# Performance work log

Measured on AMD Instinct MI355X. Metric: run time of the kernel, lower is better.

Reference implementation:

```python
import jax, jax.numpy as jnp
import numpy as np

EPS = 1e-5
TAU = 2.0

# Heaviside spike with spikingjelly's default Sigmoid surrogate gradient (alpha=4)
@jax.custom_vjp
def spike(x):
    return (x >= 0.0).astype(x.dtype)

def _spike_fwd(x):
    return (x >= 0.0).astype(x.dtype), x

def _spike_bwd(x, g):
    a = 4.0
    s = jax.nn.sigmoid(a * x)
    return (g * a * s * (1.0 - s),)

spike.defvjp(_spike_fwd, _spike_bwd)

def lif(x_seq, v_th, v_reset):
    """Multi-step LIF (decay_input=True, detach_reset=True). v_reset=None -> soft reset."""
    def step(v, x):
        if v_reset is None:
            v = v + (x - v) / TAU
        else:
            v = v + (x - (v - v_reset)) / TAU
        s = spike(v - v_th)
        sd = jax.lax.stop_gradient(s)  # detach_reset=True
        if v_reset is None:
            v = v - sd * v_th
        else:
            v = (1.0 - sd) * v + sd * v_reset
        return v, s
    _, s_seq = jax.lax.scan(step, jnp.zeros_like(x_seq[0]), x_seq)
    return s_seq

def conv2d(x, w, groups=1):
    return jax.lax.conv_general_dilated(x, w, (1, 1), 'VALID',
        dimension_numbers=('NCHW', 'OIHW', 'NCHW'), feature_group_count=groups)

def bn(x, p):
    # p: [4, C] = (weight, bias, running_mean, running_var); inference-mode BN
    w, b, m, v = p
    inv = w * jax.lax.rsqrt(v + EPS)
    return x * inv[None, :, None, None] + (b - m * inv)[None, :, None, None]

def bn_pad(x, p):
    # BNAndPadLayer(pad_pixels=1): BN then pad 1px border with the BN of zeros
    y = bn(x, p)
    w, b, m, v = p
    pv = (b - m * w * jax.lax.rsqrt(v + EPS))[None, :, None, None]
    y = jnp.pad(y, ((0, 0), (0, 0), (1, 1), (1, 1)))
    y = y.at[:, :, :1, :].set(pv)
    y = y.at[:, :, -1:, :].set(pv)
    y = y.at[:, :, :, :1].set(pv)
    y = y.at[:, :, :, -1:].set(pv)
    return y

def repconv(x, w1, bn1, dw, pw, bn2):
    y = conv2d(x, w1)                       # 1x1 in->in
    y = bn_pad(y, bn1)                      # BN + 1px pad
    y = conv2d(y, dw, groups=dw.shape[0])   # depthwise 3x3, valid
    y = conv2d(y, pw)                       # 1x1 in->out
    return bn(y, bn2)

def setup_inputs() -> dict:
    T, B, C, H, W = 4, 16, 384, 32, 32
    key = jax.random.key(0)
    ks = iter(jax.random.split(key, 32))
    def bn_params(c):
        k1, k2, k3, k4 = jax.random.split(next(ks), 4)
        return jnp.stack([
            1.0 + 0.1 * jax.random.normal(k1, (c,)),
            0.1 * jax.random.normal(k2, (c,)),
            0.1 * jax.random.normal(k3, (c,)),
            jax.random.uniform(k4, (c,), minval=0.5, maxval=1.5)]).astype(jnp.float32)
    def conv_w(shape, fan_in):
        return (jax.random.normal(next(ks), shape) / np.sqrt(fan_in)).astype(jnp.float32)
    return dict(
        x=jax.random.normal(next(ks), (T, B, C, H, W), dtype=jnp.float32),
        r1_w1=conv_w((C, C, 1, 1), C),
        r1_bn1=bn_params(C),
        r1_dw=conv_w((C, 1, 3, 3), 9),
        r1_pw=conv_w((2 * C, C, 1, 1), C),
        r1_bn2=bn_params(2 * C),
        qkv_bn=bn_params(2 * C),
        r2_w1=conv_w((C, C, 1, 1), C),
        r2_bn1=bn_params(C),
        r2_dw=conv_w((C, 1, 3, 3), 9),
        r2_pw=conv_w((C, C, 1, 1), C),
        r2_bn2=bn_params(C),
        proj_bn=bn_params(C),
        scale=jnp.array([0.1], dtype=jnp.float32),
    )

def reference(x, r1_w1, r1_bn1, r1_dw, r1_pw, r1_bn2, qkv_bn,
              r2_w1, r2_bn1, r2_dw, r2_pw, r2_bn2, proj_bn, scale):
    T, B, C, H, W = x.shape
    xs = lif(x, 1.0, 0.0)                                  # shortcut_lif (hard reset)
    y = repconv(xs.reshape(T * B, C, H, W), r1_w1, r1_bn1, r1_dw, r1_pw, r1_bn2)
    y = bn(y, qkv_bn).reshape(T, B, 2 * C, H, W)           # qkv_conv outer BN
    qk, v = y[:, :, :C], y[:, :, C:]
    qk = lif(qk, 1.0, None)                                # qk_lif (soft reset)
    qk = qk.sum(axis=(-1, -2), keepdims=True)              # jit_sum over H,W -> [T,B,C,1,1]
    qk = lif(qk, 0.5, 0.0)                                 # talking_heads_lif (th=0.5, hard)
    v = lif(v, 1.0, None)                                  # v_lif (soft reset)
    out = qk * v                                           # jit_mul broadcast over H,W
    out = repconv(out.reshape(T * B, C, H, W), r2_w1, r2_bn1, r2_dw, r2_pw, r2_bn2)
    out = bn(out, proj_bn).reshape(T, B, C, H, W)          # proj_conv outer BN
    out = lif(out, 1.0, None)                              # proj_lif (soft reset)
    return out * scale
```

## Files before the change

### kernel.cpp

```cpp
#include <hip/hip_runtime.h>

typedef _Float16 f16;
typedef __attribute__((ext_vector_type(8))) _Float16 f16x8;
typedef __attribute__((ext_vector_type(4))) _Float16 f16x4;
typedef __attribute__((ext_vector_type(4))) float f32x4;

#define TT 4
#define BB 16
#define CC 384

#define SWZ(R) ((((R) & 31)) ^ ((((R) & 4)) << 2))

__device__ __forceinline__ float lif_soft(float x, float& v) {
  v = __fadd_rn(v, __fmul_rn(__fsub_rn(x, v), 0.5f));
  float s = (__fsub_rn(v, 1.0f) >= 0.0f) ? 1.0f : 0.0f;
  v = __fsub_rn(v, s);
  return s;
}
__device__ __forceinline__ float lif_hard(float x, float& v, float vth) {
  v = __fadd_rn(v, __fmul_rn(__fsub_rn(x, v), 0.5f));
  float s = (__fsub_rn(v, vth) >= 0.0f) ? 1.0f : 0.0f;
  if (s != 0.0f) v = 0.0f;
  return s;
}

__global__ __launch_bounds__(768) void k_prep(const float* __restrict__ bn1,
                                              const float* __restrict__ bn2,
                                              const float* __restrict__ qkv,
                                              const float* __restrict__ rbn1,
                                              const float* __restrict__ rbn2,
                                              const float* __restrict__ proj,
                                              float* __restrict__ par) {
  int c = threadIdx.x;
  float* s1 = par;          float* o1 = par + 384;
  float* sA = par + 768;    float* oA = par + 1536;
  float* s2 = par + 2304;   float* o2 = par + 2688;
  float* sB = par + 3072;   float* oB = par + 3456;
  if (c < 384) {
    double a = (double)bn1[c] / sqrt((double)bn1[3*384+c] + 1e-5);
    s1[c] = (float)a;
    o1[c] = (float)((double)bn1[384+c] - (double)bn1[2*384+c]*a);
    double a2 = (double)rbn1[c] / sqrt((double)rbn1[3*384+c] + 1e-5);
    s2[c] = (float)a2;
    o2[c] = (float)((double)rbn1[384+c] - (double)rbn1[2*384+c]*a2);
    double a3 = (double)rbn2[c] / sqrt((double)rbn2[3*384+c] + 1e-5);
    double b3 = (double)rbn2[384+c] - (double)rbn2[2*384+c]*a3;
    double a4 = (double)proj[c] / sqrt((double)proj[3*384+c] + 1e-5);
    double b4 = (double)proj[384+c] - (double)proj[2*384+c]*a4;
    sB[c] = (float)(a3*a4);
    oB[c] = (float)(b3*a4 + b4);
  }
  if (c < 768) {
    double a5 = (double)bn2[c] / sqrt((double)bn2[3*768+c] + 1e-5);
    double b5 = (double)bn2[768+c] - (double)bn2[2*768+c]*a5;
    double a6 = (double)qkv[c] / sqrt((double)qkv[3*768+c] + 1e-5);
    double b6 = (double)qkv[768+c] - (double)qkv[2*768+c]*a6;
    sA[c] = (float)(a5*a6);
    oA[c] = (float)(b5*a6 + b6);
  }
}

__global__ __launch_bounds__(256) void k_wsplit(const float* __restrict__ w,
                                                f16* __restrict__ wa, f16* __restrict__ wb, int n) {
  int i = blockIdx.x * 256 + threadIdx.x;
  if (i < n) {
    float x = w[i];
    f16 a = (f16)x;
    wa[i] = a;
    wb[i] = (f16)((x - (float)a) * 2048.0f);
  }
}

__global__ __launch_bounds__(256) void k_lif_in(const float* __restrict__ x, f16* __restrict__ xs) {
  __shared__ float tile[64][65];
  const int p0 = blockIdx.x * 64, c0 = blockIdx.y * 64, b = blockIdx.z;
  const int l = threadIdx.x & 63, q = threadIdx.x >> 6;
  float v[16];
  #pragma unroll
  for (int j = 0; j < 16; ++j) v[j] = 0.0f;
  for (int t = 0; t < TT; ++t) {
    __syncthreads();
    #pragma unroll
    for (int j = 0; j < 16; ++j) {
      int ci = q + j*4;
      tile[ci][l] = x[(((size_t)(t*BB + b)*CC + c0 + ci) << 10) + p0 + l];
    }
    __syncthreads();
    #pragma unroll
    for (int j = 0; j < 16; ++j) {
      int pi = q + j*4;
      float s = lif_hard(tile[l][pi], v[j], 1.0f);
      xs[((size_t)(t*BB + b)*1024 + p0 + pi)*CC + c0 + l] = (f16)s;
    }
  }
}

template<int EPI>
__device__ __forceinline__ void stage_arrT(const f16* __restrict__ g, int m0, int b_, int p0,
                                           int k0, f16* dst, int lane, int i0, int i1, bool isX) {
  #pragma unroll
  for (int i = i0; i < i1; ++i) {
    int loff = i*1024 + lane*16;
    int row = loff >> 6, col = loff & 63;
    int scol = col ^ (((row >> 1) & 3) << 4);
    int gm;
    if (EPI >= 1 && isX) gm = ((row >> 5) << 14) + (b_ << 10) + p0 + (row & 31);
    else                 gm = m0 + row;
    const char* src = (const char*)g + (size_t)gm*768 + (size_t)(k0*2) + scol;
    __builtin_amdgcn_global_load_lds((const __attribute__((address_space(1))) void*)src,
                                     (__attribute__((address_space(3))) void*)((char*)dst + i*1024),
                                     16, 0, 0);
  }
}

__device__ __forceinline__ f16x8 fragld32(const f16* arr, int row, int fq) {
  int off = row*64 + ((fq*16) ^ (((row >> 1) & 3) << 4));
  return *(const f16x8*)((const char*)arr + off);
}

template<int NP, int EPI, int GATE>
__global__ __launch_bounds__(256, 2) void k_gemm(const f16* __restrict__ X1, const f16* __restrict__ X2,
    const f16* __restrict__ Wa, const f16* __restrict__ Wb,
    const float* __restrict__ scale, const float* __restrict__ bias,
    float* __restrict__ out0, const float* __restrict__ out1,
    const f16* __restrict__ gatep, f16* __restrict__ sOut, f16* __restrict__ part) {
  constexpr int ARR = (NP == 3) ? 4 : 3;
  __shared__ __align__(16) f16 lds[2*ARR*4096];
  const int gx = gridDim.x;
  const int bid = blockIdx.y * gx + blockIdx.x;
  const int chunk = (gx * gridDim.y) >> 3;
  const int nb = (bid & 7) * chunk + (bid >> 3);
  const int o0 = (nb % gx) * 128;
  const int mb = nb / gx;
  const int m0 = mb * 128;
  const int b_ = mb >> 5, p0 = (mb & 31) << 5;
  const int lane = threadIdx.x & 63, wid = threadIdx.x >> 6;
  const int wr = wid >> 1, wc = wid & 1;
  const int fr = lane & 15, fq = lane >> 4;
  f32x4 acc_h[4][4], acc_l[4][4];
  #pragma unroll
  for (int i = 0; i < 4; ++i)
    #pragma unroll
    for (int j = 0; j < 4; ++j) { acc_h[i][j] = (f32x4){0,0,0,0}; acc_l[i][j] = (f32x4){0,0,0,0}; }

  auto stage_all = [&](int buf, int k0) {
    f16* base = lds + buf*(ARR*4096);
    if (NP == 3) {
      if (wid == 0)      stage_arrT<EPI>(X1, m0, b_, p0, k0, base,          lane, 0, 8, true);
      else if (wid == 1) stage_arrT<EPI>(X2, m0, b_, p0, k0, base + 4096,   lane, 0, 8, true);
      else if (wid == 2) stage_arrT<EPI>(Wa, o0, b_, p0, k0, base + 2*4096, lane, 0, 8, false);
      else               stage_arrT<EPI>(Wb, o0, b_, p0, k0, base + 3*4096, lane, 0, 8, false);
    } else {
      if (wid == 0)      stage_arrT<EPI>(X1, m0, b_, p0, k0, base,          lane, 0, 4, true);
      else if (wid == 1) stage_arrT<EPI>(X1, m0, b_, p0, k0, base,          lane, 4, 8, true);
      else if (wid == 2) stage_arrT<EPI>(Wa, o0, b_, p0, k0, base + 4096,   lane, 0, 8, false);
      else               stage_arrT<EPI>(Wb, o0, b_, p0, k0, base + 2*4096, lane, 0, 8, false);
    }
  };

  const char* gbase = nullptr;
  f16x8 g8{}, gn{};
  if constexpr (GATE) {
    gbase = (const char*)gatep + (size_t)(m0 >> 10)*768 + fq*16;
    g8 = *(const f16x8*)gbase;
  }

  stage_all(0, 0);
  __syncthreads();

  for (int it = 0; it < 12; ++it) {
    const int cur = it & 1;
    if (it < 11) stage_all(cur ^ 1, (it + 1)*32);
    if constexpr (GATE) { if (it < 11) gn = *(const f16x8*)(gbase + (it + 1)*64); }
    const f16* bX1 = lds + cur*(ARR*4096);
    const f16* bW1 = (NP == 3) ? bX1 + 2*4096 : bX1 + 4096;
    const f16* bW2 = (NP == 3) ? bX1 + 3*4096 : bX1 + 2*4096;
    f16x8 a1[4], b1[4], b2[4];
    #pragma unroll
    for (int mi = 0; mi < 4; ++mi) a1[mi] = fragld32(bX1, wr*64 + mi*16 + fr, fq);
    if constexpr (GATE) {
      #pragma unroll
      for (int mi = 0; mi < 4; ++mi) a1[mi] = a1[mi] * g8;
    }
    #pragma unroll
    for (int oi = 0; oi < 4; ++oi) {
      b1[oi] = fragld32(bW1, wc*64 + oi*16 + fr, fq);
      b2[oi] = fragld32(bW2, wc*64 + oi*16 + fr, fq);
    }
    if (NP == 3) {
      const f16* bX2 = bX1 + 4096;
      f16x8 a2[4];
      #pragma unroll
      for (int mi = 0; mi < 4; ++mi) a2[mi] = fragld32(bX2, wr*64 + mi*16 + fr, fq);
      #pragma unroll
      for (int mi = 0; mi < 4; ++mi)
        #pragma unroll
        for (int oi = 0; oi < 4; ++oi) {
          acc_h[mi][oi] = __builtin_amdgcn_mfma_f32_16x16x32_f16(a1[mi], b1[oi], acc_h[mi][oi], 0, 0, 0);
          acc_l[mi][oi] = __builtin_amdgcn_mfma_f32_16x16x32_f16(a1[mi], b2[oi], acc_l[mi][oi], 0, 0, 0);
          acc_l[mi][oi] = __builtin_amdgcn_mfma_f32_16x16x32_f16(a2[mi], b1[oi], acc_l[mi][oi], 0, 0, 0);
        }
    } else {
      #pragma unroll
      for (int mi = 0; mi < 4; ++mi)
        #pragma unroll
        for (int oi = 0; oi < 4; ++oi) {
          acc_h[mi][oi] = __builtin_amdgcn_mfma_f32_16x16x32_f16(a1[mi], b1[oi], acc_h[mi][oi], 0, 0, 0);
          acc_l[mi][oi] = __builtin_amdgcn_mfma_f32_16x16x32_f16(a1[mi], b2[oi], acc_l[mi][oi], 0, 0, 0);
        }
    }
    __syncthreads();
    if constexpr (GATE) { if (it < 11) g8 = gn; }
  }

  if constexpr (EPI == 0) {
    #pragma unroll
    for (int oi = 0; oi < 4; ++oi) {
      int o = o0 + wc*64 + oi*16 + fr;
      float sc = scale[o], bi = bias[o];
      #pragma unroll
      for (int mi = 0; mi < 4; ++mi) {
        f32x4 h = acc_h[mi][oi], lo2 = acc_l[mi][oi];
        #pragma unroll
        for (int r = 0; r < 4; ++r) {
          int m = m0 + wr*64 + mi*16 + fq*4 + r;
          float y = fmaf(0.00048828125f, lo2[r], h[r]);
          out0[(size_t)m*384 + o] = fmaf(y, sc, bi);
        }
      }
    }
  } else {
    float* T = (float*)lds;
    #pragma unroll
    for (int oi = 0; oi < 4; ++oi) {
      int ol = wc*64 + oi*16 + fr;
      float sc = scale[o0 + ol], bi = bias[o0 + ol];
      #pragma unroll
      for (int mi = 0; mi < 4; ++mi) {
        f32x4 h = acc_h[mi][oi], lo2 = acc_l[mi][oi];
        #pragma unroll
        for (int r = 0; r < 4; ++r) {
          int R = wr*64 + mi*16 + fq*4 + r;
          float y = fmaf(0.00048828125f, lo2[r], h[r]);
          T[R*128 + (ol ^ SWZ(R))] = fmaf(y, sc, bi);
        }
      }
    }
    __syncthreads();
    const int tid = threadIdx.x;
    if constexpr (EPI == 1) {
      const int oc = tid & 127, ph = tid >> 7;
      if (o0 >= 384) {
        const int ocg = (o0 - 384) + oc;
        #pragma unroll
        for (int i = 0; i < 16; ++i) {
          int p = ph*16 + i;
          float v = 0.0f;
          #pragma unroll
          for (int t = 0; t < TT; ++t) {
            int R = t*32 + p;
            float s = lif_soft(T[R*128 + (oc ^ SWZ(R))], v);
            sOut[((size_t)((t*16 + b_)*1024 + p0 + p))*384 + ocg] = (f16)s;
          }
        }
      } else {
        float ps4[4] = {0,0,0,0};
        for (int i = 0; i < 16; ++i) {
          int p = ph*16 + i;
          float v = 0.0f;
          #pragma unroll
          for (int t = 0; t < TT; ++t) {
            int R = t*32 + p;
            ps4[t] += lif_soft(T[R*128 + (oc ^ SWZ(R))], v);
          }
        }
        int slice = (p0 >> 4) + ph;
        #pragma unroll
        for (int t = 0; t < TT; ++t)
          part[(((size_t)slice*4 + t)*16 + b_)*384 + o0 + oc] = (f16)ps4[t];
      }
    } else {
      const int p = tid & 31, cg = tid >> 5;
      const float gsc = out1[0];
      #pragma unroll
      for (int j = 0; j < 16; ++j) {
        int c = cg*16 + j;
        float v = 0.0f;
        #pragma unroll
        for (int t = 0; t < TT; ++t) {
          int R = t*32 + p;
          float s = lif_soft(T[R*128 + (c ^ SWZ(R))], v) * gsc;
          out0[(((size_t)(t*16 + b_)*384) + o0 + c)*1024 + p0 + p] = s;
        }
      }
    }
  }
}

__global__ __launch_bounds__(256) void k_dw(const float* __restrict__ in, const float* __restrict__ wd,
                                            const float* __restrict__ pv,
                                            f16* __restrict__ outA, f16* __restrict__ outB) {
  const int ct = blockIdx.x, h = blockIdx.y, n = blockIdx.z;
  const int cq = threadIdx.x & 15, wg = threadIdx.x >> 4;
  const int c0 = ct*64 + cq*4;
  const int w0 = wg*2;
  float w9[9][4];
  #pragma unroll
  for (int j = 0; j < 4; ++j)
    #pragma unroll
    for (int k = 0; k < 9; ++k) w9[k][j] = wd[(c0 + j)*9 + k];
  const float4 pv4 = *(const float4*)&pv[c0];
  const float* base = in + (size_t)n*1024*CC;
  float4 col[3][4];
  #pragma unroll
  for (int r = 0; r < 3; ++r)
    #pragma unroll
    for (int j = 0; j < 4; ++j) {
      int hh = h - 1 + r, ww = w0 - 1 + j;
      col[r][j] = ((unsigned)hh < 32u && (unsigned)ww < 32u)
                  ? *(const float4*)&base[(size_t)(hh*32 + ww)*CC + c0] : pv4;
    }
  #pragma unroll
  for (int wi = 0; wi < 2; ++wi) {
    float acc[4] = {0.f, 0.f, 0.f, 0.f};
    #pragma unroll
    for (int dh = 0; dh < 3; ++dh)
      #pragma unroll
      for (int dwj = 0; dwj < 3; ++dwj) {
        float4 vv = col[dh][wi + dwj];
        const float* wk = w9[dh*3 + dwj];
        acc[0] = fmaf(wk[0], vv.x, acc[0]);
        acc[1] = fmaf(wk[1], vv.y, acc[1]);
        acc[2] = fmaf(wk[2], vv.z, acc[2]);
        acc[3] = fmaf(wk[3], vv.w, acc[3]);
      }
    f16x4 a4, b4;
    #pragma unroll
    for (int j = 0; j < 4; ++j) {
      f16 a = (f16)acc[j];
      a4[j] = a;
      b4[j] = (f16)((acc[j] - (float)a) * 2048.0f);
    }
    size_t off = ((size_t)n*1024 + h*32 + w0 + wi)*CC + c0;
    *(f16x4*)&outA[off] = a4;
    *(f16x4*)&outB[off] = b4;
  }
}

__global__ __launch_bounds__(256) void k_gate(const f16* __restrict__ partial, f16* __restrict__ gate16) {
  int g = blockIdx.x*256 + threadIdx.x;
  int b = g / CC, c = g % CC;
  float sums[4];
  #pragma unroll
  for (int t = 0; t < TT; ++t) {
    float s = 0.0f;
    for (int ps = 0; ps < 64; ++ps) s += (float)partial[(((size_t)ps*4 + t)*BB + b)*CC + c];
    sums[t] = s;
  }
  float v = 0.0f;
  #pragma unroll
  for (int t = 0; t < TT; ++t)
    gate16[((size_t)(t*BB + b))*CC + c] = (f16)lif_hard(sums[t], v, 0.5f);
}

extern "C" void kernel_launch(void* const* d_in, const int* in_sizes, int n_in,
                              void* d_out, int out_size, void* d_ws, size_t ws_size,
                              hipStream_t stream) {
  const float* x      = (const float*)d_in[0];
  const float* r1_w1  = (const float*)d_in[1];
  const float* r1_bn1 = (const float*)d_in[2];
  const float* r1_dw  = (const float*)d_in[3];
  const float* r1_pw  = (const float*)d_in[4];
  const float* r1_bn2 = (const float*)d_in[5];
  const float* qkv_bn = (const float*)d_in[6];
  const float* r2_w1  = (const float*)d_in[7];
  const float* r2_bn1 = (const float*)d_in[8];
  const float* r2_dw  = (const float*)d_in[9];
  const float* r2_pw  = (const float*)d_in[10];
  const float* r2_bn2 = (const float*)d_in[11];
  const float* proj_bn= (const float*)d_in[12];
  const float* scale  = (const float*)d_in[13];

  float* ws = (float*)d_ws;
  const size_t SEG = 12582912;
  float* W0f = ws;
  float* W1  = ws + SEG;
  float* W2f = ws + 3*SEG;
  float* W3  = ws + 4*SEG;
  f16* xs  = (f16*)W0f;
  f16* p1a = (f16*)W0f;
  f16* p2b = (f16*)W0f;
  f16* p1b = (f16*)W2f;
  f16* p2a = (f16*)W2f;
  float* t1  = W1;
  f16*  s16  = (f16*)W1;
  float* t2  = W3;

  f16* wsp = (f16*)(ws + 6*SEG);
  f16* w1a = wsp,              *w1b = wsp + 147456;
  f16* pwa = wsp + 294912,     *pwb = wsp + 589824;
  f16* q1a = wsp + 884736,     *q1b = wsp + 1032192;
  f16* qpa = wsp + 1179648,    *qpb = wsp + 1327104;
  f16* partial = wsp + 1474560;
  f16* gate16  = wsp + 3047424;
  float* par = (float*)(wsp + 3072000);
  float* s1 = par,        *o1 = par + 384;
  float* sA = par + 768,  *oA = par + 1536;
  float* s2 = par + 2304, *o2 = par + 2688;
  float* sB = par + 3072, *oB = par + 3456;

  const f16* nf = (const f16*)nullptr;
  f16* nf2 = (f16*)nullptr;

  k_prep<<<1, 768, 0, stream>>>(r1_bn1, r1_bn2, qkv_bn, r2_bn1, r2_bn2, proj_bn, par);
  k_wsplit<<<576, 256, 0, stream>>>(r1_w1, w1a, w1b, 147456);
  k_wsplit<<<1152, 256, 0, stream>>>(r1_pw, pwa, pwb, 294912);
  k_wsplit<<<576, 256, 0, stream>>>(r2_w1, q1a, q1b, 147456);
  k_wsplit<<<576, 256, 0, stream>>>(r2_pw, qpa, qpb, 147456);
  k_lif_in<<<dim3(16, 6, 16), 256, 0, stream>>>(x, xs);
  k_gemm<2,0,0><<<dim3(3, 512), 256, 0, stream>>>(xs, nf, w1a, w1b, s1, o1, t1, nullptr, nf, nf2, nf2);
  k_dw<<<dim3(6, 32, 64), 256, 0, stream>>>(t1, r1_dw, o1, p1a, p1b);
  k_gemm<3,1,0><<<dim3(6, 512), 256, 0, stream>>>(p1a, p1b, pwa, pwb, sA, oA,
                                                  nullptr, nullptr, nf, s16, partial);
  k_gate<<<24, 256, 0, stream>>>(partial, gate16);
  k_gemm<2,0,1><<<dim3(3, 512), 256, 0, stream>>>(s16, nf, q1a, q1b, s2, o2, t2, nullptr, gate16, nf2, nf2);
  k_dw<<<dim3(6, 32, 64), 256, 0, stream>>>(t2, r2_dw, o2, p2a, p2b);
  k_gemm<3,2,0><<<dim3(3, 512), 256, 0, stream>>>(p2a, p2b, qpa, qpb, sB, oB,
                                                  (float*)d_out, scale, nf, nf2, nf2);
}
```

Baseline: 514.7 us.

## Split GEMM into specialized kernels with precomputed pointers and direct X2 register loads

Replaces the templated GEMM with two specialized kernels. Both precompute the global-to-LDS source pointers and fragment offsets and unroll the double-buffered k-loop by two. The three-operand variant now reads the low-part activation (X2) straight from global memory into registers instead of staging it in LDS, which cuts LDS traffic and the LDS footprint to 64KB. The four weight-split launches and the BN parameter prep are merged into one kernel, and workspace buffers are reassigned. The risk is higher register pressure and uncoalesced global loads for X2.

After: 526.4 us. 1.02x slower.

```diff
diff --git a/kernel.cpp b/kernel.cpp
--- a/kernel.cpp
+++ b/kernel.cpp
@@ -24,14 +24,28 @@
   return s;
 }
 
-__global__ __launch_bounds__(768) void k_prep(const float* __restrict__ bn1,
-                                              const float* __restrict__ bn2,
-                                              const float* __restrict__ qkv,
-                                              const float* __restrict__ rbn1,
-                                              const float* __restrict__ rbn2,
-                                              const float* __restrict__ proj,
-                                              float* __restrict__ par) {
-  int c = threadIdx.x;
+__global__ __launch_bounds__(256) void k_prep_all(const float* __restrict__ w1, const float* __restrict__ pw,
+    const float* __restrict__ q1, const float* __restrict__ qp,
+    f16* __restrict__ w1a, f16* __restrict__ w1b, f16* __restrict__ pwa, f16* __restrict__ pwb,
+    f16* __restrict__ q1a, f16* __restrict__ q1b, f16* __restrict__ qpa, f16* __restrict__ qpb,
+    const float* __restrict__ bn1, const float* __restrict__ bn2, const float* __restrict__ qkv,
+    const float* __restrict__ rbn1, const float* __restrict__ rbn2, const float* __restrict__ proj,
+    float* __restrict__ par) {
+  int bid = blockIdx.x;
+  if (bid < 2880) {
+    int i = bid*256 + threadIdx.x;
+    const float* s; f16 *da, *db; int idx;
+    if (i < 147456)      { s = w1; da = w1a; db = w1b; idx = i; }
+    else if (i < 442368) { s = pw; da = pwa; db = pwb; idx = i - 147456; }
+    else if (i < 589824) { s = q1; da = q1a; db = q1b; idx = i - 442368; }
+    else                 { s = qp; da = qpa; db = qpb; idx = i - 589824; }
+    float x = s[idx];
+    f16 a = (f16)x;
+    da[idx] = a;
+    db[idx] = (f16)((x - (float)a) * 2048.0f);
+    return;
+  }
+  int c = (bid - 2880)*256 + threadIdx.x;
   float* s1 = par;          float* o1 = par + 384;
   float* sA = par + 768;    float* oA = par + 1536;
   float* s2 = par + 2304;   float* o2 = par + 2688;
@@ -60,17 +74,6 @@
   }
 }
 
-__global__ __launch_bounds__(256) void k_wsplit(const float* __restrict__ w,
-                                                f16* __restrict__ wa, f16* __restrict__ wb, int n) {
-  int i = blockIdx.x * 256 + threadIdx.x;
-  if (i < n) {
-    float x = w[i];
-    f16 a = (f16)x;
-    wa[i] = a;
-    wb[i] = (f16)((x - (float)a) * 2048.0f);
-  }
-}
-
 __global__ __launch_bounds__(256) void k_lif_in(const float* __restrict__ x, f16* __restrict__ xs) {
   __shared__ float tile[64][65];
   const int p0 = blockIdx.x * 64, c0 = blockIdx.y * 64, b = blockIdx.z;
@@ -95,44 +98,132 @@
   }
 }
 
-template<int EPI>
-__device__ __forceinline__ void stage_arrT(const f16* __restrict__ g, int m0, int b_, int p0,
-                                           int k0, f16* dst, int lane, int i0, int i1, bool isX) {
-  #pragma unroll
-  for (int i = i0; i < i1; ++i) {
+__device__ __forceinline__ int fragoff(int row, int fq) {
+  return row*64 + ((fq*16) ^ (((row >> 1) & 3) << 4));
+}
+
+#define GLL(srcP, dstP) __builtin_amdgcn_global_load_lds( \
+    (const __attribute__((address_space(1))) void*)(srcP), \
+    (__attribute__((address_space(3))) void*)(dstP), 16, 0, 0)
+
+template<int GATE>
+__global__ __launch_bounds__(256, 2) void k_gemmA(const f16* __restrict__ X1,
+    const f16* __restrict__ Wa, const f16* __restrict__ Wb,
+    const float* __restrict__ scale, const float* __restrict__ bias,
+    float* __restrict__ out0, const f16* __restrict__ gatep) {
+  __shared__ __align__(16) f16 lds[2*3*4096];
+  char* lbase = (char*)lds;
+  const int gx = gridDim.x;
+  const int bid = blockIdx.y * gx + blockIdx.x;
+  const int chunk = (gx * gridDim.y) >> 3;
+  const int nb = (bid & 7) * chunk + (bid >> 3);
+  const int o0 = (nb % gx) * 128;
+  const int m0 = (nb / gx) * 128;
+  const int lane = threadIdx.x & 63, wid = threadIdx.x >> 6;
+  const int wr = wid >> 1, wc = wid & 1;
+  const int fr = lane & 15, fq = lane >> 4;
+  f32x4 acc_h[4][4], acc_l[4][4];
+  #pragma unroll
+  for (int i = 0; i < 4; ++i)
+    #pragma unroll
+    for (int j = 0; j < 4; ++j) { acc_h[i][j] = (f32x4){0,0,0,0}; acc_l[i][j] = (f32x4){0,0,0,0}; }
+
+  const f16* gp; int i0, nst, arr, row0;
+  if (wid == 0)      { gp = X1; arr = 0; i0 = 0; nst = 4; row0 = m0; }
+  else if (wid == 1) { gp = X1; arr = 0; i0 = 4; nst = 4; row0 = m0; }
+  else if (wid == 2) { gp = Wa; arr = 1; i0 = 0; nst = 8; row0 = o0; }
+  else               { gp = Wb; arr = 2; i0 = 0; nst = 8; row0 = o0; }
+  const char* srcp[8]; int dsto[8];
+  #pragma unroll
+  for (int j = 0; j < 8; ++j) {
+    int i = i0 + (j < nst ? j : 0);
     int loff = i*1024 + lane*16;
     int row = loff >> 6, col = loff & 63;
     int scol = col ^ (((row >> 1) & 3) << 4);
-    int gm;
-    if (EPI >= 1 && isX) gm = ((row >> 5) << 14) + (b_ << 10) + p0 + (row & 31);
-    else                 gm = m0 + row;
-    const char* src = (const char*)g + (size_t)gm*768 + (size_t)(k0*2) + scol;
-    __builtin_amdgcn_global_load_lds((const __attribute__((address_space(1))) void*)src,
-                                     (__attribute__((address_space(3))) void*)((char*)dst + i*1024),
-                                     16, 0, 0);
-  }
-}
-
-__device__ __forceinline__ f16x8 fragld32(const f16* arr, int row, int fq) {
-  int off = row*64 + ((fq*16) ^ (((row >> 1) & 3) << 4));
-  return *(const f16x8*)((const char*)arr + off);
-}
-
-template<int NP, int EPI, int GATE>
-__global__ __launch_bounds__(256, 2) void k_gemm(const f16* __restrict__ X1, const f16* __restrict__ X2,
+    srcp[j] = (const char*)gp + (size_t)(row0 + row)*768 + scol;
+    dsto[j] = arr*8192 + i*1024;
+  }
+  int offA[4], offB1[4], offB2[4];
+  #pragma unroll
+  for (int mi = 0; mi < 4; ++mi) offA[mi] = fragoff(wr*64 + mi*16 + fr, fq);
+  #pragma unroll
+  for (int oi = 0; oi < 4; ++oi) {
+    int o = fragoff(wc*64 + oi*16 + fr, fq);
+    offB1[oi] = 8192 + o;
+    offB2[oi] = 16384 + o;
+  }
+
+  const char* gb = nullptr; f16x8 gcur{}, gnxt{};
+  if constexpr (GATE) {
+    gb = (const char*)gatep + (size_t)(m0 >> 10)*768 + fq*16;
+    gcur = *(const f16x8*)gb; gb += 64;
+  }
+
+#define ISSUE_A(BUF) { _Pragma("unroll") for (int j = 0; j < 8; ++j) if (j < nst) { \
+    GLL(srcp[j], lbase + (BUF) + dsto[j]); srcp[j] += 64; } }
+#define COMPUTE_A(BUF) { f16x8 a1[4], b1[4], b2[4]; \
+    _Pragma("unroll") for (int mi = 0; mi < 4; ++mi) { \
+      a1[mi] = *(const f16x8*)(lbase + (BUF) + offA[mi]); \
+      if constexpr (GATE) a1[mi] = a1[mi] * gcur; } \
+    _Pragma("unroll") for (int oi = 0; oi < 4; ++oi) { \
+      b1[oi] = *(const f16x8*)(lbase + (BUF) + offB1[oi]); \
+      b2[oi] = *(const f16x8*)(lbase + (BUF) + offB2[oi]); } \
+    _Pragma("unroll") for (int mi = 0; mi < 4; ++mi) \
+      _Pragma("unroll") for (int oi = 0; oi < 4; ++oi) { \
+        acc_h[mi][oi] = __builtin_amdgcn_mfma_f32_16x16x32_f16(a1[mi], b1[oi], acc_h[mi][oi], 0, 0, 0); \
+        acc_l[mi][oi] = __builtin_amdgcn_mfma_f32_16x16x32_f16(a1[mi], b2[oi], acc_l[mi][oi], 0, 0, 0); } }
+
+  ISSUE_A(0);
+  __syncthreads();
+  #pragma unroll 1
+  for (int it2 = 0; it2 < 6; ++it2) {
+    ISSUE_A(24576);
+    if constexpr (GATE) { gnxt = *(const f16x8*)gb; gb += 64; }
+    COMPUTE_A(0);
+    if constexpr (GATE) gcur = gnxt;
+    __syncthreads();
+    if (it2 < 5) {
+      ISSUE_A(0);
+      if constexpr (GATE) { gnxt = *(const f16x8*)gb; gb += 64; }
+    }
+    COMPUTE_A(24576);
+    if constexpr (GATE) gcur = gnxt;
+    __syncthreads();
+  }
+#undef ISSUE_A
+#undef COMPUTE_A
+
+  #pragma unroll
+  for (int oi = 0; oi < 4; ++oi) {
+    int o = o0 + wc*64 + oi*16 + fr;
+    float sc = scale[o], bi = bias[o];
+    #pragma unroll
+    for (int mi = 0; mi < 4; ++mi) {
+      f32x4 h = acc_h[mi][oi], lo2 = acc_l[mi][oi];
+      #pragma unroll
+      for (int r = 0; r < 4; ++r) {
+        int m = m0 + wr*64 + mi*16 + fq*4 + r;
+        float y = fmaf(0.00048828125f, lo2[r], h[r]);
+        out0[(size_t)m*384 + o] = fmaf(y, sc, bi);
+      }
+    }
+  }
+}
+
+template<int EPI>
+__global__ __launch_bounds__(256, 2) void k_gemmB(const f16* __restrict__ X1, const f16* __restrict__ X2,
     const f16* __restrict__ Wa, const f16* __restrict__ Wb,
     const float* __restrict__ scale, const float* __restrict__ bias,
-    float* __restrict__ out0, const float* __restrict__ out1,
-    const f16* __restrict__ gatep, f16* __restrict__ sOut, f16* __restrict__ part) {
-  constexpr int ARR = (NP == 3) ? 4 : 3;
-  __shared__ __align__(16) f16 lds[2*ARR*4096];
+    float* __restrict__ outF, const float* __restrict__ gscale,
+    f16* __restrict__ sOut, f16* __restrict__ part) {
+  __shared__ __align__(16) f16 lds[32768];
+  char* lbase = (char*)lds;
   const int gx = gridDim.x;
   const int bid = blockIdx.y * gx + blockIdx.x;
   const int chunk = (gx * gridDim.y) >> 3;
   const int nb = (bid & 7) * chunk + (bid >> 3);
   const int o0 = (nb % gx) * 128;
   const int mb = nb / gx;
-  const int m0 = mb * 128;
   const int b_ = mb >> 5, p0 = (mb & 31) << 5;
   const int lane = threadIdx.x & 63, wid = threadIdx.x >> 6;
   const int wr = wid >> 1, wc = wid & 1;
@@ -143,155 +234,139 @@
     #pragma unroll
     for (int j = 0; j < 4; ++j) { acc_h[i][j] = (f32x4){0,0,0,0}; acc_l[i][j] = (f32x4){0,0,0,0}; }
 
-  auto stage_all = [&](int buf, int k0) {
-    f16* base = lds + buf*(ARR*4096);
-    if (NP == 3) {
-      if (wid == 0)      stage_arrT<EPI>(X1, m0, b_, p0, k0, base,          lane, 0, 8, true);
-      else if (wid == 1) stage_arrT<EPI>(X2, m0, b_, p0, k0, base + 4096,   lane, 0, 8, true);
-      else if (wid == 2) stage_arrT<EPI>(Wa, o0, b_, p0, k0, base + 2*4096, lane, 0, 8, false);
-      else               stage_arrT<EPI>(Wb, o0, b_, p0, k0, base + 3*4096, lane, 0, 8, false);
-    } else {
-      if (wid == 0)      stage_arrT<EPI>(X1, m0, b_, p0, k0, base,          lane, 0, 4, true);
-      else if (wid == 1) stage_arrT<EPI>(X1, m0, b_, p0, k0, base,          lane, 4, 8, true);
-      else if (wid == 2) stage_arrT<EPI>(Wa, o0, b_, p0, k0, base + 4096,   lane, 0, 8, false);
-      else               stage_arrT<EPI>(Wb, o0, b_, p0, k0, base + 2*4096, lane, 0, 8, false);
-    }
-  };
-
-  const char* gbase = nullptr;
-  f16x8 g8{}, gn{};
-  if constexpr (GATE) {
-    gbase = (const char*)gatep + (size_t)(m0 >> 10)*768 + fq*16;
-    g8 = *(const f16x8*)gbase;
-  }
-
-  stage_all(0, 0);
+  const char* srcp[6]; int dsto[6];
+  #pragma unroll
+  for (int j = 0; j < 6; ++j) {
+    int s = wid*6 + j, arr = s >> 3, inst = s & 7;
+    int loff = inst*1024 + lane*16;
+    int row = loff >> 6, col = loff & 63;
+    int scol = col ^ (((row >> 1) & 3) << 4);
+    const f16* gp = (arr == 0) ? X1 : (arr == 1) ? Wa : Wb;
+    int gm = (arr == 0) ? (((row >> 5) << 14) + (b_ << 10) + p0 + (row & 31)) : (o0 + row);
+    srcp[j] = (const char*)gp + (size_t)gm*768 + scol;
+    dsto[j] = arr*8192 + inst*1024;
+  }
+  const char* a2p[4];
+  #pragma unroll
+  for (int mi = 0; mi < 4; ++mi) {
+    int R = wr*64 + mi*16 + fr;
+    int gm2 = ((R >> 5) << 14) + (b_ << 10) + p0 + (R & 31);
+    a2p[mi] = (const char*)X2 + (size_t)gm2*768 + fq*16;
+  }
+  int offA[4], offB1[4], offB2[4];
+  #pragma unroll
+  for (int mi = 0; mi < 4; ++mi) offA[mi] = fragoff(wr*64 + mi*16 + fr, fq);
+  #pragma unroll
+  for (int oi = 0; oi < 4; ++oi) {
+    int o = fragoff(wc*64 + oi*16 + fr, fq);
+    offB1[oi] = 8192 + o;
+    offB2[oi] = 16384 + o;
+  }
+
+  f16x8 a2c[4], a2n[4];
+
+#define ISSUE_B(BUF) { _Pragma("unroll") for (int j = 0; j < 6; ++j) { \
+    GLL(srcp[j], lbase + (BUF) + dsto[j]); srcp[j] += 64; } }
+#define LOADA2N { _Pragma("unroll") for (int mi = 0; mi < 4; ++mi) { \
+    a2n[mi] = *(const f16x8*)a2p[mi]; a2p[mi] += 64; } }
+#define COMPUTE_B(BUF) { f16x8 a1[4], b1[4], b2[4]; \
+    _Pragma("unroll") for (int mi = 0; mi < 4; ++mi) \
+      a1[mi] = *(const f16x8*)(lbase + (BUF) + offA[mi]); \
+    _Pragma("unroll") for (int oi = 0; oi < 4; ++oi) { \
+      b1[oi] = *(const f16x8*)(lbase + (BUF) + offB1[oi]); \
+      b2[oi] = *(const f16x8*)(lbase + (BUF) + offB2[oi]); } \
+    _Pragma("unroll") for (int mi = 0; mi < 4; ++mi) \
+      _Pragma("unroll") for (int oi = 0; oi < 4; ++oi) { \
+        acc_h[mi][oi] = __builtin_amdgcn_mfma_f32_16x16x32_f16(a1[mi], b1[oi], acc_h[mi][oi], 0, 0, 0); \
+        acc_l[mi][oi] = __builtin_amdgcn_mfma_f32_16x16x32_f16(a1[mi], b2[oi], acc_l[mi][oi], 0, 0, 0); \
+        acc_l[mi][oi] = __builtin_amdgcn_mfma_f32_16x16x32_f16(a2c[mi], b1[oi], acc_l[mi][oi], 0, 0, 0); } }
+
+  ISSUE_B(0);
+  #pragma unroll
+  for (int mi = 0; mi < 4; ++mi) { a2c[mi] = *(const f16x8*)a2p[mi]; a2p[mi] += 64; }
   __syncthreads();
-
-  for (int it = 0; it < 12; ++it) {
-    const int cur = it & 1;
-    if (it < 11) stage_all(cur ^ 1, (it + 1)*32);
-    if constexpr (GATE) { if (it < 11) gn = *(const f16x8*)(gbase + (it + 1)*64); }
-    const f16* bX1 = lds + cur*(ARR*4096);
-    const f16* bW1 = (NP == 3) ? bX1 + 2*4096 : bX1 + 4096;
-    const f16* bW2 = (NP == 3) ? bX1 + 3*4096 : bX1 + 2*4096;
-    f16x8 a1[4], b1[4], b2[4];
-    #pragma unroll
-    for (int mi = 0; mi < 4; ++mi) a1[mi] = fragld32(bX1, wr*64 + mi*16 + fr, fq);
-    if constexpr (GATE) {
+  #pragma unroll 1
+  for (int it2 = 0; it2 < 6; ++it2) {
+    ISSUE_B(24576);
+    LOADA2N;
+    COMPUTE_B(0);
+    #pragma unroll
+    for (int mi = 0; mi < 4; ++mi) a2c[mi] = a2n[mi];
+    __syncthreads();
+    if (it2 < 5) {
+      ISSUE_B(0);
+      LOADA2N;
+    }
+    COMPUTE_B(24576);
+    #pragma unroll
+    for (int mi = 0; mi < 4; ++mi) a2c[mi] = a2n[mi];
+    __syncthreads();
+  }
+#undef ISSUE_B
+#undef LOADA2N
+#undef COMPUTE_B
+
+  float* T = (float*)lds;
+  #pragma unroll
+  for (int oi = 0; oi < 4; ++oi) {
+    int ol = wc*64 + oi*16 + fr;
+    float sc = scale[o0 + ol], bi = bias[o0 + ol];
+    #pragma unroll
+    for (int mi = 0; mi < 4; ++mi) {
+      f32x4 h = acc_h[mi][oi], lo2 = acc_l[mi][oi];
       #pragma unroll
-      for (int mi = 0; mi < 4; ++mi) a1[mi] = a1[mi] * g8;
-    }
-    #pragma unroll
-    for (int oi = 0; oi < 4; ++oi) {
-      b1[oi] = fragld32(bW1, wc*64 + oi*16 + fr, fq);
-      b2[oi] = fragld32(bW2, wc*64 + oi*16 + fr, fq);
-    }
-    if (NP == 3) {
-      const f16* bX2 = bX1 + 4096;
-      f16x8 a2[4];
+      for (int r = 0; r < 4; ++r) {
+        int R = wr*64 + mi*16 + fq*4 + r;
+        float y = fmaf(0.00048828125f, lo2[r], h[r]);
+        T[R*128 + (ol ^ SWZ(R))] = fmaf(y, sc, bi);
+      }
+    }
+  }
+  __syncthreads();
+  const int tid = threadIdx.x;
+  if constexpr (EPI == 1) {
+    const int oc = tid & 127, ph = tid >> 7;
+    if (o0 >= 384) {
+      const int ocg = (o0 - 384) + oc;
       #pragma unroll
-      for (int mi = 0; mi < 4; ++mi) a2[mi] = fragld32(bX2, wr*64 + mi*16 + fr, fq);
-      #pragma unroll
-      for (int mi = 0; mi < 4; ++mi)
-        #pragma unroll
-        for (int oi = 0; oi < 4; ++oi) {
-          acc_h[mi][oi] = __builtin_amdgcn_mfma_f32_16x16x32_f16(a1[mi], b1[oi], acc_h[mi][oi], 0, 0, 0);
-          acc_l[mi][oi] = __builtin_amdgcn_mfma_f32_16x16x32_f16(a1[mi], b2[oi], acc_l[mi][oi], 0, 0, 0);
-          acc_l[mi][oi] = __builtin_amdgcn_mfma_f32_16x16x32_f16(a2[mi], b1[oi], acc_l[mi][oi], 0, 0, 0);
-        }
-    } else {
-      #pragma unroll
-      for (int mi = 0; mi < 4; ++mi)
-        #pragma unroll
-        for (int oi = 0; oi < 4; ++oi) {
-          acc_h[mi][oi] = __builtin_amdgcn_mfma_f32_16x16x32_f16(a1[mi], b1[oi], acc_h[mi][oi], 0, 0, 0);
-          acc_l[mi][oi] = __builtin_amdgcn_mfma_f32_16x16x32_f16(a1[mi], b2[oi], acc_l[mi][oi], 0, 0, 0);
-        }
-    }
-    __syncthreads();
-    if constexpr (GATE) { if (it < 11) g8 = gn; }
-  }
-
-  if constexpr (EPI == 0) {
-    #pragma unroll
-    for (int oi = 0; oi < 4; ++oi) {
-      int o = o0 + wc*64 + oi*16 + fr;
-      float sc = scale[o], bi = bias[o];
-      #pragma unroll
-      for (int mi = 0; mi < 4; ++mi) {
-        f32x4 h = acc_h[mi][oi], lo2 = acc_l[mi][oi];
-        #pragma unroll
-        for (int r = 0; r < 4; ++r) {
-          int m = m0 + wr*64 + mi*16 + fq*4 + r;
-          float y = fmaf(0.00048828125f, lo2[r], h[r]);
-          out0[(size_t)m*384 + o] = fmaf(y, sc, bi);
-        }
-      }
-    }
-  } else {
-    float* T = (float*)lds;
-    #pragma unroll
-    for (int oi = 0; oi < 4; ++oi) {
-      int ol = wc*64 + oi*16 + fr;
-      float sc = scale[o0 + ol], bi = bias[o0 + ol];
-      #pragma unroll
-      for (int mi = 0; mi < 4; ++mi) {
-        f32x4 h = acc_h[mi][oi], lo2 = acc_l[mi][oi];
-        #pragma unroll
-        for (int r = 0; r < 4; ++r) {
-          int R = wr*64 + mi*16 + fq*4 + r;
-          float y = fmaf(0.00048828125f, lo2[r], h[r]);
-          T[R*128 + (ol ^ SWZ(R))] = fmaf(y, sc, bi);
-        }
-      }
-    }
-    __syncthreads();
-    const int tid = threadIdx.x;
-    if constexpr (EPI == 1) {
-      const int oc = tid & 127, ph = tid >> 7;
-      if (o0 >= 384) {
-        const int ocg = (o0 - 384) + oc;
-        #pragma unroll
-        for (int i = 0; i < 16; ++i) {
-          int p = ph*16 + i;
-          float v = 0.0f;
-          #pragma unroll
-          for (int t = 0; t < TT; ++t) {
-            int R = t*32 + p;
-            float s = lif_soft(T[R*128 + (oc ^ SWZ(R))], v);
-            sOut[((size_t)((t*16 + b_)*1024 + p0 + p))*384 + ocg] = (f16)s;
-          }
-        }
-      } else {
-        float ps4[4] = {0,0,0,0};
-        for (int i = 0; i < 16; ++i) {
-          int p = ph*16 + i;
-          float v = 0.0f;
-          #pragma unroll
-          for (int t = 0; t < TT; ++t) {
-            int R = t*32 + p;
-            ps4[t] += lif_soft(T[R*128 + (oc ^ SWZ(R))], v);
-          }
-        }
-        int slice = (p0 >> 4) + ph;
-        #pragma unroll
-        for (int t = 0; t < TT; ++t)
-          part[(((size_t)slice*4 + t)*16 + b_)*384 + o0 + oc] = (f16)ps4[t];
-      }
-    } else {
-      const int p = tid & 31, cg = tid >> 5;
-      const float gsc = out1[0];
-      #pragma unroll
-      for (int j = 0; j < 16; ++j) {
-        int c = cg*16 + j;
+      for (int i = 0; i < 16; ++i) {
+        int p = ph*16 + i;
         float v = 0.0f;
         #pragma unroll
         for (int t = 0; t < TT; ++t) {
           int R = t*32 + p;
-          float s = lif_soft(T[R*128 + (c ^ SWZ(R))], v) * gsc;
-          out0[(((size_t)(t*16 + b_)*384) + o0 + c)*1024 + p0 + p] = s;
+          float s = lif_soft(T[R*128 + (oc ^ SWZ(R))], v);
+          sOut[((size_t)((t*16 + b_)*1024 + p0 + p))*384 + ocg] = (f16)s;
         }
+      }
+    } else {
+      float ps4[4] = {0,0,0,0};
+      for (int i = 0; i < 16; ++i) {
+        int p = ph*16 + i;
+        float v = 0.0f;
+        #pragma unroll
+        for (int t = 0; t < TT; ++t) {
+          int R = t*32 + p;
+          ps4[t] += lif_soft(T[R*128 + (oc ^ SWZ(R))], v);
+        }
+      }
+      int slice = (p0 >> 4) + ph;
+      #pragma unroll
+      for (int t = 0; t < TT; ++t)
+        part[(((size_t)slice*4 + t)*16 + b_)*384 + o0 + oc] = (f16)ps4[t];
+    }
+  } else {
+    const int p = tid & 31, cg = tid >> 5;
+    const float gsc = gscale[0];
+    #pragma unroll
+    for (int j = 0; j < 16; ++j) {
+      int c = cg*16 + j;
+      float v = 0.0f;
+      #pragma unroll
+      for (int t = 0; t < TT; ++t) {
+        int R = t*32 + p;
+        float s = lif_soft(T[R*128 + (c ^ SWZ(R))], v) * gsc;
+        outF[(((size_t)(t*16 + b_)*384) + o0 + c)*1024 + p0 + p] = s;
       }
     }
   }
@@ -386,15 +461,15 @@
   float* W0f = ws;
   float* W1  = ws + SEG;
   float* W2f = ws + 3*SEG;
-  float* W3  = ws + 4*SEG;
+  float* W3f = ws + 4*SEG;
   f16* xs  = (f16*)W0f;
-  f16* p1a = (f16*)W0f;
-  f16* p2b = (f16*)W0f;
-  f16* p1b = (f16*)W2f;
+  f16* s16 = (f16*)W0f;
+  float* t1 = W1;
+  float* t2 = W1;
+  f16* p1a = (f16*)W2f;
   f16* p2a = (f16*)W2f;
-  float* t1  = W1;
-  f16*  s16  = (f16*)W1;
-  float* t2  = W3;
+  f16* p1b = (f16*)W3f;
+  f16* p2b = (f16*)W3f;
 
   f16* wsp = (f16*)(ws + 6*SEG);
   f16* w1a = wsp,              *w1b = wsp + 147456;
@@ -409,22 +484,17 @@
   float* s2 = par + 2304, *o2 = par + 2688;
   float* sB = par + 3072, *oB = par + 3456;
 
-  const f16* nf = (const f16*)nullptr;
-  f16* nf2 = (f16*)nullptr;
-
-  k_prep<<<1, 768, 0, stream>>>(r1_bn1, r1_bn2, qkv_bn, r2_bn1, r2_bn2, proj_bn, par);
-  k_wsplit<<<576, 256, 0, stream>>>(r1_w1, w1a, w1b, 147456);
-  k_wsplit<<<1152, 256, 0, stream>>>(r1_pw, pwa, pwb, 294912);
-  k_wsplit<<<576, 256, 0, stream>>>(r2_w1, q1a, q1b, 147456);
-  k_wsplit<<<576, 256, 0, stream>>>(r2_pw, qpa, qpb, 147456);
+  k_prep_all<<<2883, 256, 0, stream>>>(r1_w1, r1_pw, r2_w1, r2_pw,
+                                       w1a, w1b, pwa, pwb, q1a, q1b, qpa, qpb,
+                                       r1_bn1, r1_bn2, qkv_bn, r2_bn1, r2_bn2, proj_bn, par);
   k_lif_in<<<dim3(16, 6, 16), 256, 0, stream>>>(x, xs);
-  k_gemm<2,0,0><<<dim3(3, 512), 256, 0, stream>>>(xs, nf, w1a, w1b, s1, o1, t1, nullptr, nf, nf2, nf2);
+  k_gemmA<0><<<dim3(3, 512), 256, 0, stream>>>(xs, w1a, w1b, s1, o1, t1, nullptr);
   k_dw<<<dim3(6, 32, 64), 256, 0, stream>>>(t1, r1_dw, o1, p1a, p1b);
-  k_gemm<3,1,0><<<dim3(6, 512), 256, 0, stream>>>(p1a, p1b, pwa, pwb, sA, oA,
-                                                  nullptr, nullptr, nf, s16, partial);
+  k_gemmB<1><<<dim3(6, 512), 256, 0, stream>>>(p1a, p1b, pwa, pwb, sA, oA,
+                                               nullptr, nullptr, s16, partial);
   k_gate<<<24, 256, 0, stream>>>(partial, gate16);
-  k_gemm<2,0,1><<<dim3(3, 512), 256, 0, stream>>>(s16, nf, q1a, q1b, s2, o2, t2, nullptr, gate16, nf2, nf2);
+  k_gemmA<1><<<dim3(3, 512), 256, 0, stream>>>(s16, q1a, q1b, s2, o2, t2, gate16);
   k_dw<<<dim3(6, 32, 64), 256, 0, stream>>>(t2, r2_dw, o2, p2a, p2b);
-  k_gemm<3,2,0><<<dim3(3, 512), 256, 0, stream>>>(p2a, p2b, qpa, qpb, sB, oB,
-                                                  (float*)d_out, scale, nf, nf2, nf2);
-}
+  k_gemmB<2><<<dim3(3, 512), 256, 0, stream>>>(p2a, p2b, qpa, qpb, sB, oB,
+                                               (float*)d_out, scale, nullptr, nullptr);
+}
```
